# Optimization experiments

Hardware: AMD Instinct MI355X
Metric: run time of the kernel (lower is better)

The kernel has to match this reference:

```python
import jax, jax.numpy as jnp
import numpy as np

D = 512        # latent_dim
CD = D // 2    # complex_dim = 256
R = 8          # low-rank
UD = 32        # u_dim
NY = 50        # n_y = 2*num_prod + num_inj
SEL_IN = D + UD + 1
H = 128
EPS = 1e-5


def _bn_relu(x, g, b):
    # BatchNorm1d (training mode: batch stats, biased var) + ReLU
    mu = jnp.mean(x, axis=0)
    var = jnp.mean((x - mu) ** 2, axis=0)
    return jax.nn.relu((x - mu) / jnp.sqrt(var + EPS) * g + b)


_LAYERS = [("0", SEL_IN, H), ("1", H, H), ("2", H, D),
           ("a", D, CD), ("o", D, CD),
           ("Ur", D, CD * R), ("Ui", D, CD * R),
           ("Vr", D, CD * R), ("Vi", D, CD * R),
           ("Br", D, CD * UD), ("Bi", D, CD * UD),
           ("Cr", D, NY * CD), ("Ci", D, NY * CD),
           ("D", D, NY * UD)]


def setup_inputs() -> dict:
    key = jax.random.key(0)
    B = 2048
    inp = {}
    k0, k1, k2, kp = jax.random.split(key, 4)
    inp["zt"] = jax.random.normal(k0, (B, D), jnp.float32)
    inp["dt"] = jax.random.uniform(k1, (B, 1), jnp.float32)
    inp["ut"] = jax.random.normal(k2, (B, UD), jnp.float32)
    ks = jax.random.split(kp, len(_LAYERS))
    for (name, fin, fout), k in zip(_LAYERS, ks):
        kw, kb = jax.random.split(k)
        inp["W" + name] = jax.random.normal(kw, (fin, fout), jnp.float32) * 0.02
        inp["b" + name] = jax.random.normal(kb, (fout,), jnp.float32) * 0.02
    # BN affine params for the two hidden selector layers
    inp["g0"] = jnp.ones((H,), jnp.float32)
    inp["be0"] = jnp.zeros((H,), jnp.float32)
    inp["g1"] = jnp.ones((H,), jnp.float32)
    inp["be1"] = jnp.zeros((H,), jnp.float32)
    return inp


def _fwd(zt, dt, ut, W0, b0, g0, be0, W1, b1, g1, be1, W2, b2,
         Wa, ba, Wo, bo, WUr, bUr, WUi, bUi, WVr, bVr, WVi, bVi,
         WBr, bBr, WBi, bBi, WCr, bCr, WCi, bCi, WD, bD):
    B = zt.shape[0]
    z = jax.lax.complex(zt[:, :CD], zt[:, CD:])               # [B, CD] complex
    x = jnp.concatenate([zt, ut, dt], axis=-1)                # [B, SEL_IN]
    h = _bn_relu(x @ W0 + b0, g0, be0)
    h = _bn_relu(h @ W1 + b1, g1, be1)
    hz = h @ W2 + b2                                          # [B, D]

    alpha = -jax.nn.softplus(hz @ Wa + ba)                    # [B, CD]
    omega = hz @ Wo + bo
    Lam = jnp.exp(jax.lax.complex(alpha, omega))              # |Lam| < 1

    U = jax.lax.complex(hz @ WUr + bUr, hz @ WUi + bUi).reshape(B, CD, R)
    V = jax.lax.complex(hz @ WVr + bVr, hz @ WVi + bVi).reshape(B, CD, R)
    # U (V^H z): [B, CD]
    t = jnp.einsum('bdr,bd->br', jnp.conj(V), z)
    low_rank = jnp.einsum('bdr,br->bd', U, t)

    Bt = jax.lax.complex(hz @ WBr + bBr, hz @ WBi + bBi).reshape(B, CD, UD)
    ut_dt = ut * dt                                           # [B, UD] real
    ut_dt_c = ut_dt.astype(Lam.dtype)
    z_next = Lam * z + low_rank + jnp.einsum('bdu,bu->bd', Bt, ut_dt_c)

    Ct = jax.lax.complex(hz @ WCr + bCr, hz @ WCi + bCi).reshape(B, NY, CD)
    Dt = (hz @ WD + bD).reshape(B, NY, UD)
    yt = jnp.einsum('bnd,bd->bn', Ct, z_next).real + jnp.einsum('bnu,bu->bn', Dt, ut_dt)

    z_next_real = jnp.concatenate([z_next.real, z_next.imag], axis=-1)  # [B, D]
    return z_next_real, yt


def reference(zt, dt, ut, W0, b0, g0, be0, W1, b1, g1, be1, W2, b2,
              Wa, ba, Wo, bo, WUr, bUr, WUi, bUi, WVr, bVr, WVi, bVi,
              WBr, bBr, WBi, bBi, WCr, bCr, WCi, bCi, WD, bD):
    return _fwd(zt, dt, ut, W0, b0, g0, be0, W1, b1, g1, be1, W2, b2,
                Wa, ba, Wo, bo, WUr, bUr, WUi, bUi, WVr, bVr, WVi, bVi,
                WBr, bBr, WBi, bBi, WCr, bCr, WCi, bCi, WD, bD)
```

## Files before the change

kernel.cpp:

```cpp
#include <hip/hip_runtime.h>
#include <hip/hip_bf16.h>
#include <cstdint>
#include <cstddef>


typedef __bf16 bf16;
typedef __bf16 bf16x8 __attribute__((ext_vector_type(8)));
typedef __bf16 bf16x4 __attribute__((ext_vector_type(4)));
typedef float f32x4 __attribute__((ext_vector_type(4)));

__device__ __forceinline__ void async16(const void* g, void* l) {
  __builtin_amdgcn_global_load_lds((const __attribute__((address_space(1))) void*)g,
                                   (__attribute__((address_space(3))) void*)l, 16, 0, 0);
}

__device__ __forceinline__ bool tile_map(int NT, int& m0, int& n0) {
  int L = blockIdx.x;
  int x = L & 7, s = L >> 3;
  int nt = ((s >> 4) << 3) + x;
  if (nt >= NT) return false;
  n0 = nt << 7;
  m0 = (s & 15) << 7;
  return true;
}

__device__ __forceinline__ void gemm_wp(const bf16* __restrict__ A,
                                        const bf16* __restrict__ Bw,
                                        int m0, int n0,
                                        bf16* lds, f32x4 acc[4][4]) {
  const int tid = threadIdx.x;
  const int w = tid >> 6, l = tid & 63;
  const int wm = (w >> 1) << 6, wn = (w & 1) << 6;
  const int fr = l & 15, q = l >> 4;
  const int lr = l >> 2;
  const int koff = ((l & 3) ^ ((l >> 3) & 3)) << 3;
  const bf16* ag = A + (size_t)(m0 + wm + lr) * 512 + koff;
  const bf16* bg = Bw + (size_t)(n0 + wn + lr) * 512 + koff;
  bf16* lw = lds + (w << 13);
  const int sw = (q ^ ((fr >> 1) & 3)) << 3;

#pragma unroll
  for (int mt = 0; mt < 4; ++mt)
#pragma unroll
    for (int nt = 0; nt < 4; ++nt) { f32x4 z = {0.f, 0.f, 0.f, 0.f}; acc[mt][nt] = z; }

  auto issue = [&](int kt, int p) {
    bf16* d = lw + (p << 12);
#pragma unroll
    for (int i = 0; i < 4; ++i) async16(ag + kt + i * 8192, d + (i << 9));
#pragma unroll
    for (int i = 0; i < 4; ++i) async16(bg + kt + i * 8192, d + 2048 + (i << 9));
  };

  issue(0, 0);
#pragma unroll
  for (int it = 0; it < 16; ++it) {
    const int p = it & 1;
    if (it < 15) {
      issue((it + 1) << 5, p ^ 1);
      asm volatile("s_waitcnt vmcnt(8)" ::: "memory");
    } else {
      asm volatile("s_waitcnt vmcnt(0)" ::: "memory");
    }
    const bf16* ab = lw + (p << 12);
    const bf16* bb = ab + 2048;
    bf16x8 af[4], bfv[4];
#pragma unroll
    for (int mt = 0; mt < 4; ++mt)
      af[mt] = *(const bf16x8*)(ab + (mt * 16 + fr) * 32 + sw);
#pragma unroll
    for (int nt = 0; nt < 4; ++nt)
      bfv[nt] = *(const bf16x8*)(bb + (nt * 16 + fr) * 32 + sw);
    asm volatile("s_waitcnt lgkmcnt(0)" ::: "memory");
#pragma unroll
    for (int mt = 0; mt < 4; ++mt)
#pragma unroll
      for (int nt = 0; nt < 4; ++nt)
        acc[mt][nt] = __builtin_amdgcn_mfma_f32_16x16x32_bf16(af[mt], bfv[nt],
                                                              acc[mt][nt], 0, 0, 0);
  }
}

struct TEntry { const float* src; bf16* dst; int N, tile0, ntn; };
struct TArgs { TEntry e[11]; };

__global__ void k_transpose(TArgs a) {
  __shared__ float tile[64][65];
  int t = blockIdx.x;
  int ei = 0;
  while (ei < 10 && t >= a.e[ei + 1].tile0) ++ei;
  const TEntry E = a.e[ei];
  int lt = t - E.tile0;
  int tk = lt / E.ntn, tn = lt - tk * E.ntn;
  int k0 = tk << 6, n0 = tn << 6;
  int tid = threadIdx.x;
#pragma unroll
  for (int i = 0; i < 4; ++i) {
    int idx = tid + i * 256;
    int kk = idx >> 4, c4 = (idx & 15) << 2;
    const float4 v = *(const float4*)(E.src + (size_t)(k0 + kk) * E.N + n0 + c4);
    tile[c4 + 0][kk] = v.x; tile[c4 + 1][kk] = v.y;
    tile[c4 + 2][kk] = v.z; tile[c4 + 3][kk] = v.w;
  }
  __syncthreads();
#pragma unroll
  for (int i = 0; i < 4; ++i) {
    int idx = tid + i * 256;
    int nn = idx >> 4, k4 = (idx & 15) << 2;
    bf16x4 o;
    o[0] = (bf16)tile[nn][k4 + 0]; o[1] = (bf16)tile[nn][k4 + 1];
    o[2] = (bf16)tile[nn][k4 + 2]; o[3] = (bf16)tile[nn][k4 + 3];
    *(bf16x4*)(E.dst + (size_t)(n0 + nn) * 512 + k0 + k4) = o;
  }
}

__global__ void k_prep(const float* ba, const float* bo, const float* bVr, const float* bVi,
                       const float* bBr, const float* bBi, const float* bD,
                       const float* bUr, const float* bUi, const float* bCr, const float* bCi,
                       float* bbigA, float* bbigB, float* bbigC) {
  int i = blockIdx.x * 256 + threadIdx.x;
  if (i < 22656) {
    float v;
    if (i < 256) v = ba[i];
    else if (i < 512) v = bo[i - 256];
    else if (i < 2560) v = bVr[i - 512];
    else if (i < 4608) v = bVi[i - 2560];
    else if (i < 12800) v = bBr[i - 4608];
    else if (i < 20992) v = bBi[i - 12800];
    else if (i < 22592) v = bD[i - 20992];
    else v = 0.f;
    bbigA[i] = v;
  }
  int j = i - 22656;
  if (j >= 0 && j < 4096) bbigB[j] = (j < 2048) ? bUr[j] : bUi[j - 2048];
  int m = i - (22656 + 4096);
  if (m >= 0 && m < 25600) bbigC[m] = (m < 12800) ? bCr[m] : bCi[m - 12800];
}

__global__ void k_lin0(const float* __restrict__ zt, const float* __restrict__ dt,
                       const float* __restrict__ ut, const float* __restrict__ W0,
                       const float* __restrict__ b0, float* __restrict__ s0) {
  int i = blockIdx.x * 256 + threadIdx.x;
  int b = i >> 7, c = i & 127;
  const float* w = W0 + c;
  const float* x = zt + (size_t)b * 512;
  float acc = b0[c];
#pragma unroll 4
  for (int k = 0; k < 512; ++k) acc = fmaf(x[k], w[(size_t)k * 128], acc);
  const float* u = ut + (size_t)b * 32;
#pragma unroll
  for (int k = 0; k < 32; ++k) acc = fmaf(u[k], w[(size_t)(512 + k) * 128], acc);
  acc = fmaf(dt[b], w[(size_t)544 * 128], acc);
  s0[i] = acc;
}

__global__ void k_stats(const float* __restrict__ s, float* __restrict__ mu,
                        float* __restrict__ rstd) {
  int c = blockIdx.x;
  float sm = 0.f, sq = 0.f;
  for (int r = threadIdx.x; r < 2048; r += 256) {
    float v = s[(size_t)r * 128 + c];
    sm += v; sq += v * v;
  }
#pragma unroll
  for (int o = 32; o >= 1; o >>= 1) { sm += __shfl_down(sm, o); sq += __shfl_down(sq, o); }
  __shared__ float red[8];
  int w = threadIdx.x >> 6;
  if ((threadIdx.x & 63) == 0) { red[w] = sm; red[4 + w] = sq; }
  __syncthreads();
  if (threadIdx.x == 0) {
    float S = red[0] + red[1] + red[2] + red[3];
    float Q = red[4] + red[5] + red[6] + red[7];
    float m = S * (1.f / 2048.f);
    float var = Q * (1.f / 2048.f) - m * m;
    mu[c] = m;
    rstd[c] = rsqrtf(var + 1e-5f);
  }
}

__global__ void k_lin1(const float* __restrict__ s0, const float* __restrict__ mu,
                       const float* __restrict__ rstd, const float* __restrict__ g,
                       const float* __restrict__ be, const float* __restrict__ W1,
                       const float* __restrict__ b1, float* __restrict__ s1) {
  int i = blockIdx.x * 256 + threadIdx.x;
  int b = i >> 7, c = i & 127;
  const float* w = W1 + c;
  const float* x = s0 + (size_t)b * 128;
  float acc = b1[c];
#pragma unroll 4
  for (int k = 0; k < 128; ++k) {
    float h = fmaxf(fmaf((x[k] - mu[k]) * rstd[k], g[k], be[k]), 0.f);
    acc = fmaf(h, w[(size_t)k * 128], acc);
  }
  s1[i] = acc;
}

__global__ void k_lin2(const float* __restrict__ s1, const float* __restrict__ mu,
                       const float* __restrict__ rstd, const float* __restrict__ g,
                       const float* __restrict__ be, const float* __restrict__ W2,
                       const float* __restrict__ b2, bf16* __restrict__ hz) {
  int i = blockIdx.x * 256 + threadIdx.x;
  int b = i >> 9, c = i & 511;
  const float* w = W2 + c;
  const float* x = s1 + (size_t)b * 128;
  float acc = b2[c];
#pragma unroll 4
  for (int k = 0; k < 128; ++k) {
    float h = fmaxf(fmaf((x[k] - mu[k]) * rstd[k], g[k], be[k]), 0.f);
    acc = fmaf(h, w[(size_t)k * 512], acc);
  }
  hz[i] = (bf16)acc;
}

__global__ __launch_bounds__(256) void k_gemmA(
    const bf16* __restrict__ hz, const bf16* __restrict__ WT, const float* __restrict__ bias,
    const float* __restrict__ zt, const float* __restrict__ dt, const float* __restrict__ ut,
    float* __restrict__ pa, float* __restrict__ po,
    float* __restrict__ Bzr, float* __restrict__ Bzi,
    float* __restrict__ tbuf, float* __restrict__ ytout) {
  int m0, n0;
  if (!tile_map(177, m0, n0)) return;
  __shared__ __align__(16) bf16 lds[32768];
  f32x4 acc[4][4];
  gemm_wp(hz, WT, m0, n0, lds, acc);
  const int l = threadIdx.x & 63, w = threadIdx.x >> 6;
  const int wm = (w >> 1) << 6, wn = (w & 1) << 6;
  const int fr = l & 15, quad = l >> 4;
  const int ncol = n0 + wn;

  if (n0 < 512) {
    float* dst = (n0 < 256) ? pa : po;
    int cb = ncol - ((n0 < 256) ? 0 : 256);
#pragma unroll
    for (int mt = 0; mt < 4; ++mt)
#pragma unroll
      for (int j = 0; j < 4; ++j) {
        int b = m0 + wm + mt * 16 + quad * 4 + j;
#pragma unroll
        for (int nt = 0; nt < 4; ++nt) {
          int n = ncol + nt * 16 + fr;
          dst[(size_t)b * 256 + (cb + nt * 16 + fr)] = acc[mt][nt][j] + bias[n];
        }
      }
  } else if (n0 < 4608) {
    const bool isVr = n0 < 2560;
#pragma unroll
    for (int mt = 0; mt < 4; ++mt)
#pragma unroll
      for (int j = 0; j < 4; ++j) {
        int b = m0 + wm + mt * 16 + quad * 4 + j;
        float cre = 0.f, cim = 0.f;
#pragma unroll
        for (int nt = 0; nt < 4; ++nt) {
          int n = ncol + nt * 16 + fr;
          float v = acc[mt][nt][j] + bias[n];
          int d = ((n - 512) & 2047) >> 3;
          float zr = zt[(size_t)b * 512 + d], zi = zt[(size_t)b * 512 + 256 + d];
          if (isVr) { cre += v * zr; cim += v * zi; }
          else      { cre += v * zi; cim -= v * zr; }
        }
        cre += __shfl_xor(cre, 8);
        cim += __shfl_xor(cim, 8);
        if ((l & 8) == 0) {
          int r = fr & 7;
          atomicAdd(&tbuf[((size_t)b * 8 + r) * 2 + 0], cre);
          atomicAdd(&tbuf[((size_t)b * 8 + r) * 2 + 1], cim);
        }
      }
  } else if (n0 < 20992) {
    const bool isBr = n0 < 12800;
    float* dst = isBr ? Bzr : Bzi;
#pragma unroll
    for (int mt = 0; mt < 4; ++mt)
#pragma unroll
      for (int j = 0; j < 4; ++j) {
        int b = m0 + wm + mt * 16 + quad * 4 + j;
        float dtb = dt[b];
#pragma unroll
        for (int g = 0; g < 2; ++g) {
          float s = 0.f;
#pragma unroll
          for (int h = 0; h < 2; ++h) {
            int nt = g * 2 + h;
            int n = ncol + nt * 16 + fr;
            int base = (n - 4608) & 8191;
            float v = acc[mt][nt][j] + bias[n];
            s += v * ut[(size_t)b * 32 + (base & 31)];
          }
          s *= dtb;
          s += __shfl_xor(s, 1); s += __shfl_xor(s, 2);
          s += __shfl_xor(s, 4); s += __shfl_xor(s, 8);
          if ((l & 15) == 0) {
            int d = (((ncol + g * 32) - 4608) & 8191) >> 5;
            dst[(size_t)b * 256 + d] = s;
          }
        }
      }
  } else {
#pragma unroll
    for (int mt = 0; mt < 4; ++mt)
#pragma unroll
      for (int j = 0; j < 4; ++j) {
        int b = m0 + wm + mt * 16 + quad * 4 + j;
        float dtb = dt[b];
#pragma unroll
        for (int g = 0; g < 2; ++g) {
          float s = 0.f;
#pragma unroll
          for (int h = 0; h < 2; ++h) {
            int nt = g * 2 + h;
            int n = ncol + nt * 16 + fr;
            int base = n - 20992;
            float v = acc[mt][nt][j] + bias[n];
            s += v * ut[(size_t)b * 32 + (base & 31)];
          }
          s *= dtb;
          s += __shfl_xor(s, 1); s += __shfl_xor(s, 2);
          s += __shfl_xor(s, 4); s += __shfl_xor(s, 8);
          int nn = ((ncol + g * 32) - 20992) >> 5;
          if ((l & 15) == 0 && nn < 50) ytout[(size_t)b * 50 + nn] = s;
        }
      }
  }
}

__global__ __launch_bounds__(256) void k_gemmB(
    const bf16* __restrict__ hz, const bf16* __restrict__ WT, const float* __restrict__ bias,
    const float* __restrict__ tbuf, float* __restrict__ lr) {
  int m0, n0;
  if (!tile_map(32, m0, n0)) return;
  __shared__ __align__(16) bf16 lds[32768];
  f32x4 acc[4][4];
  gemm_wp(hz, WT, m0, n0, lds, acc);
  const int l = threadIdx.x & 63, w = threadIdx.x >> 6;
  const int wm = (w >> 1) << 6, wn = (w & 1) << 6;
  const int fr = l & 15, quad = l >> 4;
  const int ncol = n0 + wn;
  const bool isUr = n0 < 2048;
#pragma unroll
  for (int mt = 0; mt < 4; ++mt)
#pragma unroll
    for (int j = 0; j < 4; ++j) {
      int b = m0 + wm + mt * 16 + quad * 4 + j;
#pragma unroll
      for (int nt = 0; nt < 4; ++nt) {
        int n = ncol + nt * 16 + fr;
        int base = n & 2047;
        int r = base & 7, d = base >> 3;
        float v = acc[mt][nt][j] + bias[n];
        float tre = tbuf[((size_t)b * 8 + r) * 2], tim = tbuf[((size_t)b * 8 + r) * 2 + 1];
        float cre = isUr ? v * tre : -v * tim;
        float cim = isUr ? v * tim :  v * tre;
        cre += __shfl_xor(cre, 1); cre += __shfl_xor(cre, 2); cre += __shfl_xor(cre, 4);
        cim += __shfl_xor(cim, 1); cim += __shfl_xor(cim, 2); cim += __shfl_xor(cim, 4);
        if ((l & 7) == 0) {
          atomicAdd(&lr[((size_t)b * 256 + d) * 2 + 0], cre);
          atomicAdd(&lr[((size_t)b * 256 + d) * 2 + 1], cim);
        }
      }
    }
}

__global__ void k_assembleZ(const float* __restrict__ zt, const float* __restrict__ pa,
                            const float* __restrict__ po, const float* __restrict__ Bzr,
                            const float* __restrict__ Bzi, const float* __restrict__ lr,
                            float* __restrict__ zout, float* __restrict__ znr,
                            float* __restrict__ zni) {
  int i = blockIdx.x * 256 + threadIdx.x;
  int b = i >> 8, d = i & 255;
  float a = pa[i], o = po[i];
  float sp = fmaxf(a, 0.f) + log1pf(expf(-fabsf(a)));
  float mag = expf(-sp);
  float Lr = mag * cosf(o), Li = mag * sinf(o);
  float zr = zt[(size_t)b * 512 + d], zi = zt[(size_t)b * 512 + 256 + d];
  float re = fmaf(Lr, zr, -Li * zi) + Bzr[i] + lr[2 * i];
  float im = fmaf(Lr, zi,  Li * zr) + Bzi[i] + lr[2 * i + 1];
  zout[(size_t)b * 512 + d] = re;
  zout[(size_t)b * 512 + 256 + d] = im;
  znr[i] = re; zni[i] = im;
}

__global__ __launch_bounds__(256) void k_gemmC(
    const bf16* __restrict__ hz, const bf16* __restrict__ WT, const float* __restrict__ bias,
    const float* __restrict__ znr, const float* __restrict__ zni, float* __restrict__ ytout) {
  int m0, n0;
  if (!tile_map(200, m0, n0)) return;
  __shared__ __align__(16) bf16 lds[32768];
  f32x4 acc[4][4];
  gemm_wp(hz, WT, m0, n0, lds, acc);
  const int l = threadIdx.x & 63, w = threadIdx.x >> 6;
  const int wm = (w >> 1) << 6, wn = (w & 1) << 6;
  const int fr = l & 15, quad = l >> 4;
  const int ncol = n0 + wn;
  const bool isCr = n0 < 12800;
  const int nb = ncol - (isCr ? 0 : 12800);
  const int nn = nb >> 8;
#pragma unroll
  for (int mt = 0; mt < 4; ++mt)
#pragma unroll
    for (int j = 0; j < 4; ++j) {
      int b = m0 + wm + mt * 16 + quad * 4 + j;
      float s = 0.f;
#pragma unroll
      for (int nt = 0; nt < 4; ++nt) {
        int n = ncol + nt * 16 + fr;
        int d = (nb + nt * 16 + fr) & 255;
        float v = acc[mt][nt][j] + bias[n];
        s += isCr ? v * znr[(size_t)b * 256 + d] : -(v * zni[(size_t)b * 256 + d]);
      }
      s += __shfl_xor(s, 1); s += __shfl_xor(s, 2);
      s += __shfl_xor(s, 4); s += __shfl_xor(s, 8);
      if ((l & 15) == 0) atomicAdd(&ytout[(size_t)b * 50 + nn], s);
    }
}

extern "C" void kernel_launch(void* const* d_in, const int* in_sizes, int n_in,
                              void* d_out, int out_size, void* d_ws, size_t ws_size,
                              hipStream_t stream) {
  (void)in_sizes; (void)n_in; (void)out_size; (void)ws_size;
  const float* zt  = (const float*)d_in[0];
  const float* dt  = (const float*)d_in[1];
  const float* ut  = (const float*)d_in[2];
  const float* W0  = (const float*)d_in[3];  const float* b0  = (const float*)d_in[4];
  const float* W1  = (const float*)d_in[5];  const float* b1  = (const float*)d_in[6];
  const float* W2  = (const float*)d_in[7];  const float* b2  = (const float*)d_in[8];
  const float* Wa  = (const float*)d_in[9];  const float* ba  = (const float*)d_in[10];
  const float* Wo  = (const float*)d_in[11]; const float* bo  = (const float*)d_in[12];
  const float* WUr = (const float*)d_in[13]; const float* bUr = (const float*)d_in[14];
  const float* WUi = (const float*)d_in[15]; const float* bUi = (const float*)d_in[16];
  const float* WVr = (const float*)d_in[17]; const float* bVr = (const float*)d_in[18];
  const float* WVi = (const float*)d_in[19]; const float* bVi = (const float*)d_in[20];
  const float* WBr = (const float*)d_in[21]; const float* bBr = (const float*)d_in[22];
  const float* WBi = (const float*)d_in[23]; const float* bBi = (const float*)d_in[24];
  const float* WCr = (const float*)d_in[25]; const float* bCr = (const float*)d_in[26];
  const float* WCi = (const float*)d_in[27]; const float* bCi = (const float*)d_in[28];
  const float* WD  = (const float*)d_in[29]; const float* bD  = (const float*)d_in[30];
  const float* g0  = (const float*)d_in[31]; const float* be0 = (const float*)d_in[32];
  const float* g1  = (const float*)d_in[33]; const float* be1 = (const float*)d_in[34];

  char* ws = (char*)d_ws;
  bf16*  WTbig = (bf16*)(ws + 0);
  bf16*  WTU   = (bf16*)(ws + 23199744);
  bf16*  WTC   = (bf16*)(ws + 27394048);
  bf16*  hz    = (bf16*)(ws + 53608448);
  float* s0    = (float*)(ws + 55705600);
  float* s1    = (float*)(ws + 56754176);
  float* mu0   = (float*)(ws + 57802752);
  float* rstd0 = mu0 + 128;
  float* mu1   = mu0 + 256;
  float* rstd1 = mu0 + 384;
  float* bbigA = (float*)(ws + 57804800);
  float* bbigB = (float*)(ws + 57895424);
  float* bbigC = (float*)(ws + 57911808);
  float* pa    = (float*)(ws + 58014208);
  float* po    = (float*)(ws + 60111360);
  float* Bzr   = (float*)(ws + 62208512);
  float* Bzi   = (float*)(ws + 64305664);
  float* tbuf  = (float*)(ws + 66402816);
  float* lr    = (float*)(ws + 66533888);
  float* znr   = (float*)(ws + 70728192);
  float* zni   = (float*)(ws + 72825344);
  float* zout  = (float*)d_out;
  float* ytout = zout + 2048 * 512;

  k_prep<<<205, 256, 0, stream>>>(ba, bo, bVr, bVi, bBr, bBi, bD, bUr, bUi, bCr, bCi,
                                  bbigA, bbigB, bbigC);

  TArgs ta; int tile0 = 0; int idx = 0;
  auto add = [&](const float* src, bf16* dst, int N) {
    int ntn = N >> 6;
    ta.e[idx].src = src; ta.e[idx].dst = dst; ta.e[idx].N = N;
    ta.e[idx].tile0 = tile0; ta.e[idx].ntn = ntn;
    tile0 += ntn * 8; ++idx;
  };
  add(Wa,  WTbig + (size_t)0 * 512,     256);
  add(Wo,  WTbig + (size_t)256 * 512,   256);
  add(WVr, WTbig + (size_t)512 * 512,   2048);
  add(WVi, WTbig + (size_t)2560 * 512,  2048);
  add(WBr, WTbig + (size_t)4608 * 512,  8192);
  add(WBi, WTbig + (size_t)12800 * 512, 8192);
  add(WD,  WTbig + (size_t)20992 * 512, 1600);
  add(WUr, WTU,                         2048);
  add(WUi, WTU + (size_t)2048 * 512,    2048);
  add(WCr, WTC,                         12800);
  add(WCi, WTC + (size_t)12800 * 512,   12800);
  k_transpose<<<tile0, 256, 0, stream>>>(ta);

  hipMemsetAsync(tbuf, 0, 131072, stream);
  hipMemsetAsync(lr, 0, 4194304, stream);

  k_lin0<<<1024, 256, 0, stream>>>(zt, dt, ut, W0, b0, s0);
  k_stats<<<128, 256, 0, stream>>>(s0, mu0, rstd0);
  k_lin1<<<1024, 256, 0, stream>>>(s0, mu0, rstd0, g0, be0, W1, b1, s1);
  k_stats<<<128, 256, 0, stream>>>(s1, mu1, rstd1);
  k_lin2<<<4096, 256, 0, stream>>>(s1, mu1, rstd1, g1, be1, W2, b2, hz);

  k_gemmA<<<184 * 16, 256, 0, stream>>>(hz, WTbig, bbigA, zt, dt, ut,
                                        pa, po, Bzr, Bzi, tbuf, ytout);
  k_gemmB<<<32 * 16, 256, 0, stream>>>(hz, WTU, bbigB, tbuf, lr);
  k_assembleZ<<<2048, 256, 0, stream>>>(zt, pa, po, Bzr, Bzi, lr, zout, znr, zni);
  k_gemmC<<<200 * 16, 256, 0, stream>>>(hz, WTC, bbigC, znr, zni, ytout);
}
```

Baseline: 646.8 us.

## Share GEMM tiles across warps with a three-stage LDS pipeline

The GEMM mainloop changes from per-warp private A/B copies (each warp loading its own 64-row slices) to a block-shared 128x32 A and B tile that all four warps read from. Each thread issues four async loads per stage instead of eight, and the ring grows from two to three stages, kept in order by barriers. The aim is to cut duplicated global-to-LDS traffic and LDS footprint (64KB down to 48KB) and to prefetch two stages ahead. The cost is a block-wide s_barrier every k-step.

```diff
diff --git a/kernel.cpp b/kernel.cpp
--- a/kernel.cpp
+++ b/kernel.cpp
@@ -24,7 +24,7 @@
   return true;
 }
 
-__device__ __forceinline__ void gemm_wp(const bf16* __restrict__ A,
+__device__ __forceinline__ void gemm_p3(const bf16* __restrict__ A,
                                         const bf16* __restrict__ Bw,
                                         int m0, int n0,
                                         bf16* lds, f32x4 acc[4][4]) {
@@ -32,11 +32,14 @@
   const int w = tid >> 6, l = tid & 63;
   const int wm = (w >> 1) << 6, wn = (w & 1) << 6;
   const int fr = l & 15, q = l >> 4;
-  const int lr = l >> 2;
-  const int koff = ((l & 3) ^ ((l >> 3) & 3)) << 3;
-  const bf16* ag = A + (size_t)(m0 + wm + lr) * 512 + koff;
-  const bf16* bg = Bw + (size_t)(n0 + wn + lr) * 512 + koff;
-  bf16* lw = lds + (w << 13);
+
+  const int c0 = tid, c1 = tid + 256;
+  const int r0 = c0 >> 2, k0 = ((c0 & 3) ^ ((r0 >> 1) & 3)) << 3;
+  const int r1 = c1 >> 2, k1 = ((c1 & 3) ^ ((r1 >> 1) & 3)) << 3;
+  const bf16* a0 = A + (size_t)(m0 + r0) * 512 + k0;
+  const bf16* a1 = A + (size_t)(m0 + r1) * 512 + k1;
+  const bf16* b0 = Bw + (size_t)(n0 + r0) * 512 + k0;
+  const bf16* b1 = Bw + (size_t)(n0 + r1) * 512 + k1;
   const int sw = (q ^ ((fr >> 1) & 3)) << 3;
 
 #pragma unroll
@@ -45,33 +48,32 @@
     for (int nt = 0; nt < 4; ++nt) { f32x4 z = {0.f, 0.f, 0.f, 0.f}; acc[mt][nt] = z; }
 
   auto issue = [&](int kt, int p) {
-    bf16* d = lw + (p << 12);
-#pragma unroll
-    for (int i = 0; i < 4; ++i) async16(ag + kt + i * 8192, d + (i << 9));
-#pragma unroll
-    for (int i = 0; i < 4; ++i) async16(bg + kt + i * 8192, d + 2048 + (i << 9));
+    bf16* d = lds + p * 8192;
+    async16(a0 + kt, d + (c0 << 3));
+    async16(a1 + kt, d + (c1 << 3));
+    async16(b0 + kt, d + 4096 + (c0 << 3));
+    async16(b1 + kt, d + 4096 + (c1 << 3));
   };
 
   issue(0, 0);
+  issue(32, 1);
 #pragma unroll
   for (int it = 0; it < 16; ++it) {
-    const int p = it & 1;
-    if (it < 15) {
-      issue((it + 1) << 5, p ^ 1);
-      asm volatile("s_waitcnt vmcnt(8)" ::: "memory");
-    } else {
-      asm volatile("s_waitcnt vmcnt(0)" ::: "memory");
-    }
-    const bf16* ab = lw + (p << 12);
-    const bf16* bb = ab + 2048;
+    const int p = it % 3;
+    if (it < 14) asm volatile("s_waitcnt vmcnt(4)" ::: "memory");
+    else         asm volatile("s_waitcnt vmcnt(0)" ::: "memory");
+    asm volatile("s_barrier" ::: "memory");
+    const bf16* ab = lds + p * 8192;
+    const bf16* bb = ab + 4096;
     bf16x8 af[4], bfv[4];
 #pragma unroll
     for (int mt = 0; mt < 4; ++mt)
-      af[mt] = *(const bf16x8*)(ab + (mt * 16 + fr) * 32 + sw);
+      af[mt] = *(const bf16x8*)(ab + (wm + mt * 16 + fr) * 32 + sw);
 #pragma unroll
     for (int nt = 0; nt < 4; ++nt)
-      bfv[nt] = *(const bf16x8*)(bb + (nt * 16 + fr) * 32 + sw);
+      bfv[nt] = *(const bf16x8*)(bb + (wn + nt * 16 + fr) * 32 + sw);
     asm volatile("s_waitcnt lgkmcnt(0)" ::: "memory");
+    if (it + 2 < 16) issue((it + 2) << 5, (it + 2) % 3);
 #pragma unroll
     for (int mt = 0; mt < 4; ++mt)
 #pragma unroll
@@ -220,9 +222,9 @@
     float* __restrict__ tbuf, float* __restrict__ ytout) {
   int m0, n0;
   if (!tile_map(177, m0, n0)) return;
-  __shared__ __align__(16) bf16 lds[32768];
+  __shared__ __align__(16) bf16 lds[24576];
   f32x4 acc[4][4];
-  gemm_wp(hz, WT, m0, n0, lds, acc);
+  gemm_p3(hz, WT, m0, n0, lds, acc);
   const int l = threadIdx.x & 63, w = threadIdx.x >> 6;
   const int wm = (w >> 1) << 6, wn = (w & 1) << 6;
   const int fr = l & 15, quad = l >> 4;
@@ -329,9 +331,9 @@
     const float* __restrict__ tbuf, float* __restrict__ lr) {
   int m0, n0;
   if (!tile_map(32, m0, n0)) return;
-  __shared__ __align__(16) bf16 lds[32768];
+  __shared__ __align__(16) bf16 lds[24576];
   f32x4 acc[4][4];
-  gemm_wp(hz, WT, m0, n0, lds, acc);
+  gemm_p3(hz, WT, m0, n0, lds, acc);
   const int l = threadIdx.x & 63, w = threadIdx.x >> 6;
   const int wm = (w >> 1) << 6, wn = (w & 1) << 6;
   const int fr = l & 15, quad = l >> 4;
@@ -385,9 +387,9 @@
     const float* __restrict__ znr, const float* __restrict__ zni, float* __restrict__ ytout) {
   int m0, n0;
   if (!tile_map(200, m0, n0)) return;
-  __shared__ __align__(16) bf16 lds[32768];
+  __shared__ __align__(16) bf16 lds[24576];
   f32x4 acc[4][4];
-  gemm_wp(hz, WT, m0, n0, lds, acc);
+  gemm_p3(hz, WT, m0, n0, lds, acc);
   const int l = threadIdx.x & 63, w = threadIdx.x >> 6;
   const int wm = (w >> 1) << 6, wn = (w & 1) << 6;
   const int fr = l & 15, quad = l >> 4;
```

New measurement: 586.1 us. 9.4% less time.
